# Kernel tuning notes

Measured on AMD Instinct MI355X. Metric: run time of the kernel, lower is better.

## Reference

```python
import jax, jax.numpy as jnp
import numpy as np

B, NV, RN, SN = 1, 4, 1024, 128
H = W = 256
C_FEAT = 32   # img_feat_dim
D_VIEW = 32   # view transformer d_model
PE_D = 8      # PE_d_hid
D_RAY = D_VIEW + PE_D  # 40
NHEAD = 8
EPS_LN = 1e-5


def _layernorm(x, g, b):
    m = x.mean(-1, keepdims=True)
    v = ((x - m) ** 2).mean(-1, keepdims=True)
    return (x - m) * jax.lax.rsqrt(v + EPS_LN) * g + b


def _linear_attention(q, k, v):
    # LoFTR kernelized linear attention; q,k,v: (n, L, h, d)
    Q = jax.nn.elu(q) + 1.0
    K = jax.nn.elu(k) + 1.0
    L = v.shape[1]
    KV = jnp.einsum('nshd,nshv->nhdv', K, v / L)
    Z = 1.0 / (jnp.einsum('nlhd,nhd->nlh', Q, K.sum(axis=1)) + 1e-6)
    return jnp.einsum('nlhd,nhdv,nlh->nlhv', Q, KV, Z) * L


def _loftr_self_layer(x, Wq, Wk, Wv, Wm, g1, b1, W1, W2, g2, b2):
    # LoFTREncoderLayer with self-attention (x is both query and source)
    n, L, d = x.shape
    dim = d // NHEAD
    q = (x @ Wq).reshape(n, L, NHEAD, dim)
    k = (x @ Wk).reshape(n, L, NHEAD, dim)
    v = (x @ Wv).reshape(n, L, NHEAD, dim)
    msg = _linear_attention(q, k, v).reshape(n, L, d) @ Wm
    msg = _layernorm(msg, g1, b1)
    msg = jax.nn.relu(jnp.concatenate([x, msg], -1) @ W1) @ W2
    msg = _layernorm(msg, g2, b2)
    return x + msg


def _grid_sample_2d(img, pix):
    # img: (N,C,H,W); pix: (N,RN,SN,2) in pixel coords.
    # bilinear, align_corners=True, zero padding; mask = in-bounds.
    N, C, Hh, Ww = img.shape
    x, y = pix[..., 0], pix[..., 1]
    mask = ((x >= 0) & (x <= Ww - 1) & (y >= 0) & (y <= Hh - 1)).astype(img.dtype)
    x0 = jnp.floor(x)
    y0 = jnp.floor(y)
    flat = img.reshape(N, C, Hh * Ww)

    def gather(ix, iy):
        valid = ((ix >= 0) & (ix < Ww) & (iy >= 0) & (iy < Hh)).astype(img.dtype)
        idx = (jnp.clip(iy, 0, Hh - 1) * Ww + jnp.clip(ix, 0, Ww - 1)).astype(jnp.int32)
        out = jnp.take_along_axis(flat, idx.reshape(N, 1, -1), axis=2)
        return out.reshape(N, C, ix.shape[1], ix.shape[2]) * valid[:, None]

    wx1 = x - x0
    wy1 = y - y0
    out = (gather(x0, y0) * ((1 - wx1) * (1 - wy1))[:, None]
           + gather(x0 + 1, y0) * (wx1 * (1 - wy1))[:, None]
           + gather(x0, y0 + 1) * ((1 - wx1) * wy1)[:, None]
           + gather(x0 + 1, y0 + 1) * (wx1 * wy1)[:, None])
    return out, mask


def _order_posenc(d_hid, n):
    pos = np.arange(n)[:, None].astype(np.float64)
    j = np.arange(d_hid)[None, :]
    tab = pos / np.power(10000.0, 2 * (j // 2) / d_hid)
    tab[:, 0::2] = np.sin(tab[:, 0::2])
    tab[:, 1::2] = np.cos(tab[:, 1::2])
    return jnp.asarray(tab, dtype=jnp.float32)


def _forward(point3D, source_imgs, source_imgs_feat, ref_pose_inv, source_poses_inv,
             source_poses, view_token,
             vt_Wq, vt_Wk, vt_Wv, vt_Wm, vt_g1, vt_b1, vt_W1, vt_W2, vt_g2, vt_b2,
             rt_Wq, rt_Wk, rt_Wv, rt_Wm, rt_g1, rt_b1, rt_W1, rt_W2, rt_g2, rt_b2,
             dm_W1, dm_b1, dm_W2, dm_b2, dm_W3, dm_b3,
             rw_W1, rw_b1, rw_W2, rw_b2, rw_W3, rw_b3):
    b, nv, _, h, w = source_imgs.shape
    _, rn, sn, _ = point3D.shape

    # relative viewing directions (B,NV,RN,SN,3)
    v1 = point3D - ref_pose_inv[:, None, None, :3, -1]
    v2 = point3D[:, None] - source_poses_inv[:, :, None, None, :3, -1]
    v1 = v1 / jnp.linalg.norm(v1, axis=-1, keepdims=True)
    v2 = v2 / jnp.linalg.norm(v2, axis=-1, keepdims=True)
    dir_relative = v1[:, None] - v2

    # project points into all source views: (B,NV,3,RN,SN)
    pts_h = jnp.concatenate([point3D, jnp.ones_like(point3D[..., :1])], -1)
    pip = jnp.einsum('bnij,brsj->bnirs', source_poses, pts_h)[:, :, :3]
    mask_valid_depth = (pip[:, :, 2] > 0).astype(point3D.dtype)
    pix = pip[:, :, :2] / pip[:, :, 2:3]
    grid = jnp.moveaxis(pix, 2, -1).reshape(b * nv, rn, sn, 2)

    feat_s, mask = _grid_sample_2d(source_imgs_feat.reshape(b * nv, -1, h, w), grid)
    rgb_s, _ = _grid_sample_2d(source_imgs.reshape(b * nv, -1, h, w), grid)
    mask = mask.reshape(b, nv, rn, sn) * mask_valid_depth

    # per-point multi-view tokens: (B*RN*SN, NV, C)
    x = feat_s.reshape(b, nv, -1, rn, sn).transpose(0, 3, 4, 1, 2).reshape(b * rn * sn, nv, -1)
    tok = jnp.broadcast_to(view_token, (x.shape[0], 1, view_token.shape[-1]))
    x = jnp.concatenate([tok, x], axis=1)  # prepend view token -> L = NV+1
    x = _loftr_self_layer(x, vt_Wq, vt_Wk, vt_Wv, vt_Wm, vt_g1, vt_b1, vt_W1, vt_W2, vt_g2, vt_b2)

    x1 = jnp.moveaxis(x, 1, 0)          # (NV+1, B*RN*SN, C)
    view_feature = x1[1:]
    x = x1[0].reshape(b * rn, sn, -1)   # token output per sample along ray

    pe = _order_posenc(PE_D, sn)        # (SN, 8)
    x = jnp.concatenate([x, jnp.broadcast_to(pe, (b * rn, sn, PE_D))], -1)
    x = _loftr_self_layer(x, rt_Wq, rt_Wk, rt_Wv, rt_Wm, rt_g1, rt_b1, rt_W1, rt_W2, rt_g2, rt_b2)

    hdm = jax.nn.relu(x @ dm_W1 + dm_b1)
    hdm = jax.nn.relu(hdm @ dm_W2 + dm_b2)
    srdf = hdm @ dm_W3 + dm_b3           # (B*RN, SN, 1)

    # radiance blending weights over views
    vf = view_feature.reshape(nv, b, rn, sn, -1).transpose(1, 2, 3, 0, 4)  # (B,RN,SN,NV,C)
    dr = dir_relative.transpose(0, 2, 3, 1, 4)                             # (B,RN,SN,NV,3)
    xw = jnp.concatenate([vf, dr], -1)
    xw = jax.nn.relu(xw @ rw_W1 + rw_b1)
    xw = jax.nn.relu(xw @ rw_W2 + rw_b2)
    xw = xw @ rw_W3 + rw_b3                                                # (B,RN,SN,NV,1)
    m = mask.transpose(0, 2, 3, 1)[..., None]
    xw = jnp.where(m == 0, -1e9, xw)
    weight = jax.nn.softmax(xw, axis=-2)
    w_bn = weight[..., 0].transpose(0, 3, 1, 2)[:, :, None]                # (B,NV,1,RN,SN)
    radiance = (rgb_s.reshape(b, nv, 3, rn, sn) * w_bn).sum(axis=1)        # (B,3,RN,SN)
    radiance = radiance.transpose(0, 2, 3, 1).reshape(b * rn * sn, 3)
    return radiance, srdf, pip


def setup_inputs() -> dict:
    key = jax.random.key(0)
    ks = jax.random.split(key, 4)
    u = jax.random.uniform(ks[0], (B, RN, SN, 3), dtype=jnp.float32)
    point3D = jnp.concatenate([u[..., :2] - 0.5, u[..., 2:] + 1.0], -1)  # x,y in [-.5,.5], z in [1,2]
    source_imgs = jax.random.normal(ks[1], (B, NV, 3, H, W), dtype=jnp.float32) * 0.5
    source_imgs_feat = jax.random.normal(ks[2], (B, NV, C_FEAT, H, W), dtype=jnp.float32) * 0.5

    f = 200.0
    P = np.array([[f, 0, W / 2, 0], [0, f, H / 2, 0], [0, 0, 1, 0], [0, 0, 0, 1]], np.float32)
    source_poses = jnp.asarray(np.broadcast_to(P, (B, NV, 4, 4)).copy())
    ref_pose_inv = jnp.asarray(np.broadcast_to(np.eye(4, dtype=np.float32), (B, 4, 4)).copy())
    spi = np.broadcast_to(np.eye(4, dtype=np.float32), (B, NV, 4, 4)).copy()
    spi[:, :, 0, 3] = np.linspace(-0.2, 0.2, NV, dtype=np.float32)  # camera centers
    source_poses_inv = jnp.asarray(spi)

    pk = jax.random.split(ks[3], 20)

    def lin(k, i, o):
        return jax.random.normal(k, (i, o), dtype=jnp.float32) * 0.05

    d, dr = D_VIEW, D_RAY
    params = dict(
        view_token=jax.random.normal(pk[0], (1, d), dtype=jnp.float32),
        vt_Wq=lin(pk[1], d, d), vt_Wk=lin(pk[2], d, d), vt_Wv=lin(pk[3], d, d), vt_Wm=lin(pk[4], d, d),
        vt_g1=jnp.ones(d), vt_b1=jnp.zeros(d),
        vt_W1=lin(pk[5], 2 * d, 2 * d), vt_W2=lin(pk[6], 2 * d, d),
        vt_g2=jnp.ones(d), vt_b2=jnp.zeros(d),
        rt_Wq=lin(pk[7], dr, dr), rt_Wk=lin(pk[8], dr, dr), rt_Wv=lin(pk[9], dr, dr), rt_Wm=lin(pk[10], dr, dr),
        rt_g1=jnp.ones(dr), rt_b1=jnp.zeros(dr),
        rt_W1=lin(pk[11], 2 * dr, 2 * dr), rt_W2=lin(pk[12], 2 * dr, dr),
        rt_g2=jnp.ones(dr), rt_b2=jnp.zeros(dr),
        dm_W1=lin(pk[13], dr, 32), dm_b1=jnp.zeros(32),
        dm_W2=lin(pk[14], 32, 16), dm_b2=jnp.zeros(16),
        dm_W3=lin(pk[15], 16, 1), dm_b3=jnp.zeros(1),
        rw_W1=lin(pk[16], d + 3, 16), rw_b1=jnp.zeros(16),
        rw_W2=lin(pk[17], 16, 8), rw_b2=jnp.zeros(8),
        rw_W3=lin(pk[18], 8, 1), rw_b3=jnp.zeros(1),
    )
    out = dict(point3D=point3D, source_imgs=source_imgs, source_imgs_feat=source_imgs_feat,
               ref_pose_inv=ref_pose_inv, source_poses_inv=source_poses_inv,
               source_poses=source_poses)
    out.update(params)
    return out


def reference(point3D, source_imgs, source_imgs_feat, ref_pose_inv, source_poses_inv,
              source_poses, view_token,
              vt_Wq, vt_Wk, vt_Wv, vt_Wm, vt_g1, vt_b1, vt_W1, vt_W2, vt_g2, vt_b2,
              rt_Wq, rt_Wk, rt_Wv, rt_Wm, rt_g1, rt_b1, rt_W1, rt_W2, rt_g2, rt_b2,
              dm_W1, dm_b1, dm_W2, dm_b2, dm_W3, dm_b3,
              rw_W1, rw_b1, rw_W2, rw_b2, rw_W3, rw_b3):
    return _forward(point3D, source_imgs, source_imgs_feat, ref_pose_inv, source_poses_inv,
                    source_poses, view_token,
                    vt_Wq, vt_Wk, vt_Wv, vt_Wm, vt_g1, vt_b1, vt_W1, vt_W2, vt_g2, vt_b2,
                    rt_Wq, rt_Wk, rt_Wv, rt_Wm, rt_g1, rt_b1, rt_W1, rt_W2, rt_g2, rt_b2,
                    dm_W1, dm_b1, dm_W2, dm_b2, dm_W3, dm_b3,
                    rw_W1, rw_b1, rw_W2, rw_b2, rw_W3, rw_b3)
```

## Files before the change

kernel.cpp:

```cpp
#include <hip/hip_runtime.h>
#include <math.h>

#define NPTS   131072
#define NVIEW  4
#define IMH    256
#define IMW    256

#define WS_FEATT   0u
#define WS_IMGT    8388608u
#define WS_X1      9437184u
#define WS_XR      26214400u
#define WS_MSG     31457280u
#define WS_RGB     36700160u
#define WS_DIR     38273024u
#define WS_MASK    39845888u

__device__ __forceinline__ float elup1(float t) { return t > 0.f ? t + 1.f : expf(t); }

__global__ __launch_bounds__(256) void k0_transpose(
    const float* __restrict__ feat, const float* __restrict__ img,
    float* __restrict__ featT, float* __restrict__ imgT)
{
    int tid = blockIdx.x * 256 + threadIdx.x;
    int v = tid >> 16, pix = tid & 65535;
    float buf[32];
#pragma unroll
    for (int c = 0; c < 32; ++c)
        buf[c] = feat[((size_t)(v * 32 + c) << 16) + pix];
    float4* dst = (float4*)(featT + ((size_t)tid << 5));
#pragma unroll
    for (int q = 0; q < 8; ++q)
        dst[q] = make_float4(buf[4*q], buf[4*q+1], buf[4*q+2], buf[4*q+3]);
    float4 rgb;
    rgb.x = img[((size_t)(v * 3 + 0) << 16) + pix];
    rgb.y = img[((size_t)(v * 3 + 1) << 16) + pix];
    rgb.z = img[((size_t)(v * 3 + 2) << 16) + pix];
    rgb.w = 0.f;
    *(float4*)(imgT + ((size_t)tid << 2)) = rgb;
}

__global__ __launch_bounds__(256) void k1_geom_sample(
    const float* __restrict__ p3d, const float* __restrict__ rpi,
    const float* __restrict__ spi, const float* __restrict__ sp,
    const float* __restrict__ featT, const float* __restrict__ imgT,
    float* __restrict__ x1, float* __restrict__ rgbw,
    float* __restrict__ dirw, float* __restrict__ maskw,
    float* __restrict__ outpip)
{
    int tid = blockIdx.x * 256 + threadIdx.x;
    int p = tid >> 2, v = tid & 3;
    float X = p3d[p * 3 + 0], Y = p3d[p * 3 + 1], Z = p3d[p * 3 + 2];

    float a0 = X - rpi[3], a1 = Y - rpi[7], a2 = Z - rpi[11];
    float na = sqrtf(a0 * a0 + a1 * a1 + a2 * a2);
    a0 /= na; a1 /= na; a2 /= na;
    const float* sv = spi + v * 16;
    float b0 = X - sv[3], b1 = Y - sv[7], b2 = Z - sv[11];
    float nb = sqrtf(b0 * b0 + b1 * b1 + b2 * b2);
    b0 /= nb; b1 /= nb; b2 /= nb;
    dirw[(size_t)p * 12 + v * 3 + 0] = a0 - b0;
    dirw[(size_t)p * 12 + v * 3 + 1] = a1 - b1;
    dirw[(size_t)p * 12 + v * 3 + 2] = a2 - b2;

    const float* P = sp + v * 16;
    float pip0 = P[0] * X + P[1] * Y + P[2]  * Z + P[3];
    float pip1 = P[4] * X + P[5] * Y + P[6]  * Z + P[7];
    float pip2 = P[8] * X + P[9] * Y + P[10] * Z + P[11];
    outpip[(size_t)(v * 3 + 0) * NPTS + p] = pip0;
    outpip[(size_t)(v * 3 + 1) * NPTS + p] = pip1;
    outpip[(size_t)(v * 3 + 2) * NPTS + p] = pip2;

    float gx = pip0 / pip2, gy = pip1 / pip2;
    float inb = (gx >= 0.f && gx <= 255.f && gy >= 0.f && gy <= 255.f) ? 1.f : 0.f;
    float mvd = pip2 > 0.f ? 1.f : 0.f;
    maskw[(size_t)p * 4 + v] = inb * mvd;

    float x0f = floorf(gx), y0f = floorf(gy);
    float wx = gx - x0f, wy = gy - y0f;
    int ix0 = (int)x0f, iy0 = (int)y0f;
    float tw[4] = { (1.f-wx)*(1.f-wy), wx*(1.f-wy), (1.f-wx)*wy, wx*wy };
    int tdx[4] = { 0, 1, 0, 1 };
    int tdy[4] = { 0, 0, 1, 1 };

    float facc[32];
#pragma unroll
    for (int c = 0; c < 32; ++c) facc[c] = 0.f;
    float r0 = 0.f, r1 = 0.f, r2 = 0.f;

#pragma unroll
    for (int tno = 0; tno < 4; ++tno) {
        int ix = ix0 + tdx[tno], iy = iy0 + tdy[tno];
        float valid = (ix >= 0 && ix < IMW && iy >= 0 && iy < IMH) ? 1.f : 0.f;
        int cx = min(max(ix, 0), IMW - 1), cy = min(max(iy, 0), IMH - 1);
        float wgt = tw[tno] * valid;
        size_t base = ((size_t)v << 16) + ((size_t)cy << 8) + (size_t)cx;
        const float4* fp = (const float4*)(featT + base * 32);
#pragma unroll
        for (int q = 0; q < 8; ++q) {
            float4 f4 = fp[q];
            facc[4*q+0] += f4.x * wgt; facc[4*q+1] += f4.y * wgt;
            facc[4*q+2] += f4.z * wgt; facc[4*q+3] += f4.w * wgt;
        }
        float4 rp = *(const float4*)(imgT + base * 4);
        r0 += rp.x * wgt; r1 += rp.y * wgt; r2 += rp.z * wgt;
    }

    float4* xd = (float4*)(x1 + ((size_t)p * 4 + v) * 32);
#pragma unroll
    for (int q = 0; q < 8; ++q)
        xd[q] = make_float4(facc[4*q], facc[4*q+1], facc[4*q+2], facc[4*q+3]);
    rgbw[(size_t)p * 12 + v * 3 + 0] = r0;
    rgbw[(size_t)p * 12 + v * 3 + 1] = r1;
    rgbw[(size_t)p * 12 + v * 3 + 2] = r2;
}

__global__ __launch_bounds__(256) void k2_loftr1(
    float* __restrict__ x1g, const float* __restrict__ vtok,
    const float* __restrict__ Wq, const float* __restrict__ Wk,
    const float* __restrict__ Wv, const float* __restrict__ Wm,
    const float* __restrict__ g1, const float* __restrict__ b1,
    const float* __restrict__ W1, const float* __restrict__ W2,
    const float* __restrict__ g2, const float* __restrict__ b2,
    float* __restrict__ xr)
{
    __shared__ float sm[10400 + 8 * 640];
    int tid = threadIdx.x;
    for (int i = tid; i < 1024; i += 256) {
        sm[i] = Wq[i]; sm[1024 + i] = Wk[i]; sm[2048 + i] = Wv[i]; sm[3072 + i] = Wm[i];
    }
    for (int i = tid; i < 4096; i += 256) sm[4096 + i] = W1[i];
    for (int i = tid; i < 2048; i += 256) sm[8192 + i] = W2[i];
    if (tid < 32) {
        sm[10240 + tid] = g1[tid]; sm[10272 + tid] = b1[tid];
        sm[10304 + tid] = g2[tid]; sm[10336 + tid] = b2[tid];
        sm[10368 + tid] = vtok[tid];
    }
    __syncthreads();

    int pp = tid >> 5, c = tid & 31;
    float* S = sm + 10400 + pp * 640;

    for (int g = blockIdx.x; g < NPTS / 8; g += gridDim.x) {
        int p = g * 8 + pp;
        S[c] = sm[10368 + c];
#pragma unroll
        for (int vv = 0; vv < 4; ++vv)
            S[(1 + vv) * 32 + c] = x1g[((size_t)p * 4 + vv) * 32 + c];
        __syncthreads();

        {
            float qa[5], ka[5], va[5];
#pragma unroll
            for (int l = 0; l < 5; ++l) { qa[l] = 0.f; ka[l] = 0.f; va[l] = 0.f; }
            for (int kk = 0; kk < 32; ++kk) {
                float wq = sm[kk * 32 + c], wk = sm[1024 + kk * 32 + c], wv = sm[2048 + kk * 32 + c];
#pragma unroll
                for (int l = 0; l < 5; ++l) {
                    float xv = S[l * 32 + kk];
                    qa[l] += xv * wq; ka[l] += xv * wk; va[l] += xv * wv;
                }
            }
#pragma unroll
            for (int l = 0; l < 5; ++l) {
                S[160 + l * 32 + c] = elup1(qa[l]);
                S[320 + l * 32 + c] = elup1(ka[l]);
                S[480 + l * 32 + c] = va[l];
            }
        }
        __syncthreads();

        {
            int hb = (c >> 2) << 2;
            float Vl[5], Ke[5][4];
#pragma unroll
            for (int s2 = 0; s2 < 5; ++s2) {
                Vl[s2] = S[480 + s2 * 32 + c];
#pragma unroll
                for (int e = 0; e < 4; ++e) Ke[s2][e] = S[320 + s2 * 32 + hb + e];
            }
            float kv[4] = {0,0,0,0}, ks[4] = {0,0,0,0};
#pragma unroll
            for (int s2 = 0; s2 < 5; ++s2)
#pragma unroll
                for (int e = 0; e < 4; ++e) { kv[e] += Ke[s2][e] * Vl[s2]; ks[e] += Ke[s2][e]; }
#pragma unroll
            for (int l = 0; l < 5; ++l) {
                float q0 = S[160 + l * 32 + hb], q1 = S[160 + l * 32 + hb + 1];
                float q2 = S[160 + l * 32 + hb + 2], q3 = S[160 + l * 32 + hb + 3];
                float den = q0*ks[0] + q1*ks[1] + q2*ks[2] + q3*ks[3] + 1e-6f;
                float o   = q0*kv[0] + q1*kv[1] + q2*kv[2] + q3*kv[3];
                S[480 + l * 32 + c] = o / den;
            }
        }
        __syncthreads();

        {
            float ma[5] = {0,0,0,0,0};
            for (int kk = 0; kk < 32; ++kk) {
                float w = sm[3072 + kk * 32 + c];
#pragma unroll
                for (int l = 0; l < 5; ++l) ma[l] += S[480 + l * 32 + kk] * w;
            }
#pragma unroll
            for (int l = 0; l < 5; ++l) {
                float s1 = ma[l], s2v = ma[l] * ma[l];
#pragma unroll
                for (int off = 16; off > 0; off >>= 1) {
                    s1  += __shfl_xor(s1,  off, 32);
                    s2v += __shfl_xor(s2v, off, 32);
                }
                float m  = s1 * (1.f / 32.f);
                float va = s2v * (1.f / 32.f) - m * m;
                float rs = rsqrtf(va + 1e-5f);
                S[160 + l * 32 + c] = (ma[l] - m) * rs * sm[10240 + c] + sm[10272 + c];
            }
        }
        __syncthreads();

        {
            float hA[5] = {0,0,0,0,0}, hB[5] = {0,0,0,0,0};
            for (int kk = 0; kk < 32; ++kk) {
                float wa = sm[4096 + kk * 64 + c],        wb2 = sm[4096 + kk * 64 + c + 32];
                float wc = sm[4096 + (32 + kk) * 64 + c], wd  = sm[4096 + (32 + kk) * 64 + c + 32];
#pragma unroll
                for (int l = 0; l < 5; ++l) {
                    float xv = S[l * 32 + kk], mv = S[160 + l * 32 + kk];
                    hA[l] += xv * wa + mv * wc;
                    hB[l] += xv * wb2 + mv * wd;
                }
            }
#pragma unroll
            for (int l = 0; l < 5; ++l) {
                S[320 + l * 64 + c]      = fmaxf(hA[l], 0.f);
                S[320 + l * 64 + c + 32] = fmaxf(hB[l], 0.f);
            }
        }
        __syncthreads();

        {
            float oa[5] = {0,0,0,0,0};
            for (int kk = 0; kk < 64; ++kk) {
                float w = sm[8192 + kk * 32 + c];
#pragma unroll
                for (int l = 0; l < 5; ++l) oa[l] += S[320 + l * 64 + kk] * w;
            }
#pragma unroll
            for (int l = 0; l < 5; ++l) {
                float s1 = oa[l], s2v = oa[l] * oa[l];
#pragma unroll
                for (int off = 16; off > 0; off >>= 1) {
                    s1  += __shfl_xor(s1,  off, 32);
                    s2v += __shfl_xor(s2v, off, 32);
                }
                float m  = s1 * (1.f / 32.f);
                float va = s2v * (1.f / 32.f) - m * m;
                float rs = rsqrtf(va + 1e-5f);
                float y  = S[l * 32 + c] + (oa[l] - m) * rs * sm[10304 + c] + sm[10336 + c];
                if (l == 0) xr[(size_t)p * 40 + c] = y;
                else        x1g[((size_t)p * 4 + (l - 1)) * 32 + c] = y;
            }
            if (c < 8) {
                int sidx = p & 127;
                float den = (c < 2) ? 1.f : (c < 4) ? 10.f : (c < 6) ? 100.f : 1000.f;
                float arg = (float)sidx / den;
                xr[(size_t)p * 40 + 32 + c] = (c & 1) ? cosf(arg) : sinf(arg);
            }
        }
        __syncthreads();
    }
}

__global__ __launch_bounds__(320) void k3a_attn(
    const float* __restrict__ xr,
    const float* __restrict__ Wq, const float* __restrict__ Wk,
    const float* __restrict__ Wv, const float* __restrict__ Wm,
    const float* __restrict__ g1, const float* __restrict__ b1,
    float* __restrict__ msg)
{
    __shared__ float kb[5120];
    __shared__ float vb[5120];
    __shared__ float wb[1600];
    __shared__ float kvb[200];
    __shared__ float ksb[40];
    int t = threadIdx.x, r = blockIdx.x;
    const float* xbase = xr + (size_t)r * 5120;
    int lg = t / 40, c = t % 40;

    for (int i = t; i < 1600; i += 320) wb[i] = Wk[i];
    __syncthreads();
    {
        float acc[16];
#pragma unroll
        for (int i = 0; i < 16; ++i) acc[i] = 0.f;
        for (int kk = 0; kk < 40; ++kk) {
            float w = wb[kk * 40 + c];
#pragma unroll
            for (int i = 0; i < 16; ++i) acc[i] += xbase[(lg * 16 + i) * 40 + kk] * w;
        }
#pragma unroll
        for (int i = 0; i < 16; ++i) kb[(lg * 16 + i) * 40 + c] = elup1(acc[i]);
    }
    __syncthreads();
    for (int i = t; i < 1600; i += 320) wb[i] = Wv[i];
    __syncthreads();
    {
        float acc[16];
#pragma unroll
        for (int i = 0; i < 16; ++i) acc[i] = 0.f;
        for (int kk = 0; kk < 40; ++kk) {
            float w = wb[kk * 40 + c];
#pragma unroll
            for (int i = 0; i < 16; ++i) acc[i] += xbase[(lg * 16 + i) * 40 + kk] * w;
        }
#pragma unroll
        for (int i = 0; i < 16; ++i) vb[(lg * 16 + i) * 40 + c] = acc[i];
    }
    __syncthreads();
    if (t < 200) {
        int h = t / 25, e = (t / 5) % 5, d = t % 5;
        float kv = 0.f, ks = 0.f;
        for (int s2 = 0; s2 < 128; ++s2) {
            float kvv = kb[s2 * 40 + h * 5 + e];
            float vv  = vb[s2 * 40 + h * 5 + d];
            kv += kvv * vv; ks += kvv;
        }
        kvb[t] = kv;
        if (d == 0) ksb[h * 5 + e] = ks;
    }
    __syncthreads();
    for (int i = t; i < 1600; i += 320) wb[i] = Wq[i];
    __syncthreads();
    {
        float acc[16];
#pragma unroll
        for (int i = 0; i < 16; ++i) acc[i] = 0.f;
        for (int kk = 0; kk < 40; ++kk) {
            float w = wb[kk * 40 + c];
#pragma unroll
            for (int i = 0; i < 16; ++i) acc[i] += xbase[(lg * 16 + i) * 40 + kk] * w;
        }
#pragma unroll
        for (int i = 0; i < 16; ++i) kb[(lg * 16 + i) * 40 + c] = elup1(acc[i]);
    }
    __syncthreads();
    {
        int h = c / 5, d = c % 5;
#pragma unroll 4
        for (int i = 0; i < 16; ++i) {
            int l = lg * 16 + i;
            float den = 1e-6f, o = 0.f;
#pragma unroll
            for (int e = 0; e < 5; ++e) {
                float q = kb[l * 40 + h * 5 + e];
                den += q * ksb[h * 5 + e];
                o   += q * kvb[h * 25 + e * 5 + d];
            }
            vb[l * 40 + c] = o / den;
        }
    }
    __syncthreads();
    for (int i = t; i < 1600; i += 320) wb[i] = Wm[i];
    __syncthreads();
    {
        float acc[16];
#pragma unroll
        for (int i = 0; i < 16; ++i) acc[i] = 0.f;
        for (int kk = 0; kk < 40; ++kk) {
            float w = wb[kk * 40 + c];
#pragma unroll
            for (int i = 0; i < 16; ++i) acc[i] += vb[(lg * 16 + i) * 40 + kk] * w;
        }
#pragma unroll
        for (int i = 0; i < 16; ++i) kb[(lg * 16 + i) * 40 + c] = acc[i];
    }
    __syncthreads();
    if (t < 128) {
        float s1 = 0.f, s2v = 0.f;
        for (int j = 0; j < 40; ++j) { float x = kb[t * 40 + j]; s1 += x; s2v += x * x; }
        float m = s1 * (1.f / 40.f), va = s2v * (1.f / 40.f) - m * m;
        float rs = rsqrtf(va + 1e-5f);
        for (int j = 0; j < 40; ++j)
            msg[((size_t)r * 128 + t) * 40 + j] = (kb[t * 40 + j] - m) * rs * g1[j] + b1[j];
    }
}

__global__ __launch_bounds__(320) void k3b_ffn(
    float* __restrict__ xr, const float* __restrict__ msg,
    const float* __restrict__ W1, const float* __restrict__ W2,
    const float* __restrict__ g2, const float* __restrict__ b2)
{
    __shared__ float hb[10240];
    __shared__ float wb[3200];
    int t = threadIdx.x, r = blockIdx.x;
    int lg = t / 40, c = t % 40;
    const float* xbase = xr + (size_t)r * 5120;
    const float* mbase = msg + (size_t)r * 5120;

    float hA[16], hB[16];
#pragma unroll
    for (int i = 0; i < 16; ++i) { hA[i] = 0.f; hB[i] = 0.f; }

    for (int i = t; i < 3200; i += 320) wb[i] = W1[i];
    __syncthreads();
    for (int kk = 0; kk < 40; ++kk) {
        float wa = wb[kk * 80 + c], wbb = wb[kk * 80 + c + 40];
#pragma unroll
        for (int i = 0; i < 16; ++i) {
            float xv = xbase[(lg * 16 + i) * 40 + kk];
            hA[i] += xv * wa; hB[i] += xv * wbb;
        }
    }
    __syncthreads();
    for (int i = t; i < 3200; i += 320) wb[i] = W1[3200 + i];
    __syncthreads();
    for (int kk = 0; kk < 40; ++kk) {
        float wa = wb[kk * 80 + c], wbb = wb[kk * 80 + c + 40];
#pragma unroll
        for (int i = 0; i < 16; ++i) {
            float mv = mbase[(lg * 16 + i) * 40 + kk];
            hA[i] += mv * wa; hB[i] += mv * wbb;
        }
    }
#pragma unroll
    for (int i = 0; i < 16; ++i) {
        hb[(lg * 16 + i) * 80 + c]      = fmaxf(hA[i], 0.f);
        hb[(lg * 16 + i) * 80 + c + 40] = fmaxf(hB[i], 0.f);
    }
    __syncthreads();
    for (int i = t; i < 3200; i += 320) wb[i] = W2[i];
    __syncthreads();
    float oa[16];
#pragma unroll
    for (int i = 0; i < 16; ++i) oa[i] = 0.f;
    for (int kk = 0; kk < 80; ++kk) {
        float w = wb[kk * 40 + c];
#pragma unroll
        for (int i = 0; i < 16; ++i) oa[i] += hb[(lg * 16 + i) * 80 + kk] * w;
    }
    __syncthreads();
#pragma unroll
    for (int i = 0; i < 16; ++i) hb[(lg * 16 + i) * 40 + c] = oa[i];
    __syncthreads();
    if (t < 128) {
        float s1 = 0.f, s2v = 0.f;
        for (int j = 0; j < 40; ++j) { float x = hb[t * 40 + j]; s1 += x; s2v += x * x; }
        float m = s1 * (1.f / 40.f), va = s2v * (1.f / 40.f) - m * m;
        float rs = rsqrtf(va + 1e-5f);
        for (int j = 0; j < 40; ++j) {
            float y = xbase[t * 40 + j] + (hb[t * 40 + j] - m) * rs * g2[j] + b2[j];
            xr[(size_t)r * 5120 + t * 40 + j] = y;
        }
    }
}

__global__ __launch_bounds__(256) void k4_dm(
    const float* __restrict__ xr,
    const float* __restrict__ W1, const float* __restrict__ b1,
    const float* __restrict__ W2, const float* __restrict__ b2,
    const float* __restrict__ W3, const float* __restrict__ b3,
    float* __restrict__ out1)
{
    __shared__ float s[1857];
    int t = threadIdx.x;
    for (int i = t; i < 1280; i += 256) s[i] = W1[i];
    if (t < 32) s[1280 + t] = b1[t];
    for (int i = t; i < 512; i += 256) s[1312 + i] = W2[i];
    if (t < 16) { s[1824 + t] = b2[t]; s[1840 + t] = W3[t]; }
    if (t == 0) s[1856] = b3[0];
    __syncthreads();

    int p = blockIdx.x * 256 + t;
    float x[40];
    const float4* xp = (const float4*)(xr + (size_t)p * 40);
#pragma unroll
    for (int i = 0; i < 10; ++i) {
        float4 v4 = xp[i];
        x[4*i] = v4.x; x[4*i+1] = v4.y; x[4*i+2] = v4.z; x[4*i+3] = v4.w;
    }
    float h1[32];
#pragma unroll
    for (int j = 0; j < 32; ++j) h1[j] = s[1280 + j];
    for (int k = 0; k < 40; ++k) {
        float xv = x[k];
#pragma unroll
        for (int j = 0; j < 32; ++j) h1[j] += xv * s[k * 32 + j];
    }
#pragma unroll
    for (int j = 0; j < 32; ++j) h1[j] = fmaxf(h1[j], 0.f);
    float h2[16];
#pragma unroll
    for (int j = 0; j < 16; ++j) h2[j] = s[1824 + j];
    for (int k = 0; k < 32; ++k) {
        float hv = h1[k];
#pragma unroll
        for (int j = 0; j < 16; ++j) h2[j] += hv * s[1312 + k * 16 + j];
    }
    float o = s[1856];
#pragma unroll
    for (int j = 0; j < 16; ++j) o += fmaxf(h2[j], 0.f) * s[1840 + j];
    out1[p] = o;
}

__global__ __launch_bounds__(256) void k5_rw(
    const float* __restrict__ vf, const float* __restrict__ dirw,
    const float* __restrict__ maskw, const float* __restrict__ rgbw,
    const float* __restrict__ W1, const float* __restrict__ b1,
    const float* __restrict__ W2, const float* __restrict__ b2,
    const float* __restrict__ W3, const float* __restrict__ b3,
    float* __restrict__ out0)
{
    __shared__ float s[721];
    int t = threadIdx.x;
    for (int i = t; i < 560; i += 256) s[i] = W1[i];
    if (t < 16) s[560 + t] = b1[t];
    if (t < 128) s[576 + t] = W2[t];
    if (t < 8) { s[704 + t] = b2[t]; s[712 + t] = W3[t]; }
    if (t == 0) s[720] = b3[0];
    __syncthreads();

    int p = blockIdx.x * 256 + t;
    float xw[4];
#pragma unroll
    for (int v = 0; v < 4; ++v) {
        float in[35];
        const float4* vp = (const float4*)(vf + ((size_t)p * 4 + v) * 32);
#pragma unroll
        for (int q = 0; q < 8; ++q) {
            float4 f4 = vp[q];
            in[4*q] = f4.x; in[4*q+1] = f4.y; in[4*q+2] = f4.z; in[4*q+3] = f4.w;
        }
        in[32] = dirw[(size_t)p * 12 + v * 3 + 0];
        in[33] = dirw[(size_t)p * 12 + v * 3 + 1];
        in[34] = dirw[(size_t)p * 12 + v * 3 + 2];
        float h1[16];
#pragma unroll
        for (int j = 0; j < 16; ++j) h1[j] = s[560 + j];
        for (int k = 0; k < 35; ++k) {
            float xv = in[k];
#pragma unroll
            for (int j = 0; j < 16; ++j) h1[j] += xv * s[k * 16 + j];
        }
        float h2[8];
#pragma unroll
        for (int j = 0; j < 8; ++j) h2[j] = s[704 + j];
        for (int k = 0; k < 16; ++k) {
            float hv = fmaxf(h1[k], 0.f);
#pragma unroll
            for (int j = 0; j < 8; ++j) h2[j] += hv * s[576 + k * 8 + j];
        }
        float o = s[720];
#pragma unroll
        for (int j = 0; j < 8; ++j) o += fmaxf(h2[j], 0.f) * s[712 + j];
        xw[v] = (maskw[(size_t)p * 4 + v] == 0.f) ? -1e9f : o;
    }
    float m = fmaxf(fmaxf(xw[0], xw[1]), fmaxf(xw[2], xw[3]));
    float e0 = expf(xw[0] - m), e1 = expf(xw[1] - m), e2 = expf(xw[2] - m), e3 = expf(xw[3] - m);
    float inv = 1.f / (e0 + e1 + e2 + e3);
    float w4[4] = { e0 * inv, e1 * inv, e2 * inv, e3 * inv };
    float r0 = 0.f, r1 = 0.f, r2 = 0.f;
#pragma unroll
    for (int v = 0; v < 4; ++v) {
        r0 += rgbw[(size_t)p * 12 + v * 3 + 0] * w4[v];
        r1 += rgbw[(size_t)p * 12 + v * 3 + 1] * w4[v];
        r2 += rgbw[(size_t)p * 12 + v * 3 + 2] * w4[v];
    }
    out0[(size_t)p * 3 + 0] = r0;
    out0[(size_t)p * 3 + 1] = r1;
    out0[(size_t)p * 3 + 2] = r2;
}

extern "C" void kernel_launch(void* const* d_in, const int* in_sizes, int n_in,
                              void* d_out, int out_size, void* d_ws, size_t ws_size,
                              hipStream_t stream) {
    (void)in_sizes; (void)n_in; (void)out_size; (void)ws_size;
    const float* p3d   = (const float*)d_in[0];
    const float* imgs  = (const float*)d_in[1];
    const float* feat  = (const float*)d_in[2];
    const float* rpi   = (const float*)d_in[3];
    const float* spi   = (const float*)d_in[4];
    const float* sp    = (const float*)d_in[5];
    const float* vtok  = (const float*)d_in[6];
    const float* vtWq  = (const float*)d_in[7];
    const float* vtWk  = (const float*)d_in[8];
    const float* vtWv  = (const float*)d_in[9];
    const float* vtWm  = (const float*)d_in[10];
    const float* vtg1  = (const float*)d_in[11];
    const float* vtb1  = (const float*)d_in[12];
    const float* vtW1  = (const float*)d_in[13];
    const float* vtW2  = (const float*)d_in[14];
    const float* vtg2  = (const float*)d_in[15];
    const float* vtb2  = (const float*)d_in[16];
    const float* rtWq  = (const float*)d_in[17];
    const float* rtWk  = (const float*)d_in[18];
    const float* rtWv  = (const float*)d_in[19];
    const float* rtWm  = (const float*)d_in[20];
    const float* rtg1  = (const float*)d_in[21];
    const float* rtb1  = (const float*)d_in[22];
    const float* rtW1  = (const float*)d_in[23];
    const float* rtW2  = (const float*)d_in[24];
    const float* rtg2  = (const float*)d_in[25];
    const float* rtb2  = (const float*)d_in[26];
    const float* dmW1  = (const float*)d_in[27];
    const float* dmb1  = (const float*)d_in[28];
    const float* dmW2  = (const float*)d_in[29];
    const float* dmb2  = (const float*)d_in[30];
    const float* dmW3  = (const float*)d_in[31];
    const float* dmb3  = (const float*)d_in[32];
    const float* rwW1  = (const float*)d_in[33];
    const float* rwb1  = (const float*)d_in[34];
    const float* rwW2  = (const float*)d_in[35];
    const float* rwb2  = (const float*)d_in[36];
    const float* rwW3  = (const float*)d_in[37];
    const float* rwb3  = (const float*)d_in[38];

    float* out  = (float*)d_out;
    float* out0 = out;
    float* out1 = out + 393216;
    float* out2 = out + 524288;

    float* ws    = (float*)d_ws;
    float* featT = ws + WS_FEATT;
    float* imgT  = ws + WS_IMGT;
    float* x1    = ws + WS_X1;
    float* xr    = ws + WS_XR;
    float* msg   = ws + WS_MSG;
    float* rgbw  = ws + WS_RGB;
    float* dirw  = ws + WS_DIR;
    float* maskw = ws + WS_MASK;

    k0_transpose<<<dim3(1024), dim3(256), 0, stream>>>(feat, imgs, featT, imgT);
    k1_geom_sample<<<dim3(2048), dim3(256), 0, stream>>>(p3d, rpi, spi, sp, featT, imgT,
                                                         x1, rgbw, dirw, maskw, out2);
    k2_loftr1<<<dim3(2048), dim3(256), 0, stream>>>(x1, vtok, vtWq, vtWk, vtWv, vtWm,
                                                    vtg1, vtb1, vtW1, vtW2, vtg2, vtb2, xr);
    k3a_attn<<<dim3(1024), dim3(320), 0, stream>>>(xr, rtWq, rtWk, rtWv, rtWm, rtg1, rtb1, msg);
    k3b_ffn<<<dim3(1024), dim3(320), 0, stream>>>(xr, msg, rtW1, rtW2, rtg2, rtb2);
    k4_dm<<<dim3(512), dim3(256), 0, stream>>>(xr, dmW1, dmb1, dmW2, dmb2, dmW3, dmb3, out1);
    k5_rw<<<dim3(512), dim3(256), 0, stream>>>(x1, dirw, maskw, rgbw,
                                               rwW1, rwb1, rwW2, rwb2, rwW3, rwb3, out0);
}
```

Baseline: 1.219 ms.

## Restructure view-transformer kernel to one token row per thread with register accumulators

The LoFTR view-transformer kernel changes from one point per 32-thread group, with weights staged in shared memory and a barrier between every stage, to a layout where each thread owns one token row (24 points × 5 tokens per 128-thread block). Each thread keeps all 32/64 output channels in registers, and weights are read straight from global memory as uniform values that can go through scalar loads. Layernorm reductions become in-register sums instead of shuffles, and there are far fewer barriers. The cost is heavy register pressure (64-wide accumulators plus q and o arrays) and 8 idle threads per block, which may lower occupancy or cause spills.

```diff
diff --git a/kernel.cpp b/kernel.cpp
--- a/kernel.cpp
+++ b/kernel.cpp
@@ -114,159 +114,276 @@
     rgbw[(size_t)p * 12 + v * 3 + 2] = r2;
 }
 
-__global__ __launch_bounds__(256) void k2_loftr1(
+#define K2_BLK 128
+#define K2_PTS 24
+
+__global__ __launch_bounds__(K2_BLK) void k2_loftr1(
     float* __restrict__ x1g, const float* __restrict__ vtok,
     const float* __restrict__ Wq, const float* __restrict__ Wk,
     const float* __restrict__ Wv, const float* __restrict__ Wm,
-    const float* __restrict__ g1, const float* __restrict__ b1,
+    const float* __restrict__ g1v, const float* __restrict__ b1v,
     const float* __restrict__ W1, const float* __restrict__ W2,
-    const float* __restrict__ g2, const float* __restrict__ b2,
+    const float* __restrict__ g2v, const float* __restrict__ b2v,
     float* __restrict__ xr)
 {
-    __shared__ float sm[10400 + 8 * 640];
-    int tid = threadIdx.x;
-    for (int i = tid; i < 1024; i += 256) {
-        sm[i] = Wq[i]; sm[1024 + i] = Wk[i]; sm[2048 + i] = Wv[i]; sm[3072 + i] = Wm[i];
-    }
-    for (int i = tid; i < 4096; i += 256) sm[4096 + i] = W1[i];
-    for (int i = tid; i < 2048; i += 256) sm[8192 + i] = W2[i];
-    if (tid < 32) {
-        sm[10240 + tid] = g1[tid]; sm[10272 + tid] = b1[tid];
-        sm[10304 + tid] = g2[tid]; sm[10336 + tid] = b2[tid];
-        sm[10368 + tid] = vtok[tid];
-    }
-    __syncthreads();
-
-    int pp = tid >> 5, c = tid & 31;
-    float* S = sm + 10400 + pp * 640;
-
-    for (int g = blockIdx.x; g < NPTS / 8; g += gridDim.x) {
-        int p = g * 8 + pp;
-        S[c] = sm[10368 + c];
-#pragma unroll
-        for (int vv = 0; vv < 4; ++vv)
-            S[(1 + vv) * 32 + c] = x1g[((size_t)p * 4 + vv) * 32 + c];
-        __syncthreads();
-
-        {
-            float qa[5], ka[5], va[5];
-#pragma unroll
-            for (int l = 0; l < 5; ++l) { qa[l] = 0.f; ka[l] = 0.f; va[l] = 0.f; }
-            for (int kk = 0; kk < 32; ++kk) {
-                float wq = sm[kk * 32 + c], wk = sm[1024 + kk * 32 + c], wv = sm[2048 + kk * 32 + c];
-#pragma unroll
-                for (int l = 0; l < 5; ++l) {
-                    float xv = S[l * 32 + kk];
-                    qa[l] += xv * wq; ka[l] += xv * wk; va[l] += xv * wv;
+    __shared__ float xs[8 * K2_BLK * 4];
+    __shared__ float kvs[8192];
+
+    int t = threadIdx.x;
+    int pl = t / 5, l = t - pl * 5;
+    bool act = (t < K2_PTS * 5);
+    if (!act) { pl = 0; l = 0; }
+    int p = blockIdx.x * K2_PTS + pl;
+    bool valid = act && (p < NPTS);
+    int pload = p < NPTS ? p : NPTS - 1;
+
+    {
+        float4 xrow[8];
+        if (l == 0) {
+            const float4* sv = (const float4*)vtok;
+#pragma unroll
+            for (int g = 0; g < 8; ++g) xrow[g] = sv[g];
+        } else {
+            const float4* sv = (const float4*)(x1g + ((size_t)pload * 4 + (l - 1)) * 32);
+#pragma unroll
+            for (int g = 0; g < 8; ++g) xrow[g] = sv[g];
+        }
+#pragma unroll
+        for (int g = 0; g < 8; ++g)
+            *(float4*)&xs[(g * K2_BLK + t) * 4] = xrow[g];
+    }
+
+    {
+        float acc[32];
+#pragma unroll
+        for (int j = 0; j < 32; ++j) acc[j] = 0.f;
+#pragma unroll 2
+        for (int g = 0; g < 8; ++g) {
+            float4 xv = *(const float4*)&xs[(g * K2_BLK + t) * 4];
+            const float* w0 = Wk + g * 128;
+#pragma unroll
+            for (int j = 0; j < 32; ++j) acc[j] = fmaf(xv.x, w0[j],      acc[j]);
+#pragma unroll
+            for (int j = 0; j < 32; ++j) acc[j] = fmaf(xv.y, w0[32 + j], acc[j]);
+#pragma unroll
+            for (int j = 0; j < 32; ++j) acc[j] = fmaf(xv.z, w0[64 + j], acc[j]);
+#pragma unroll
+            for (int j = 0; j < 32; ++j) acc[j] = fmaf(xv.w, w0[96 + j], acc[j]);
+        }
+        if (act) {
+            float* krow = &kvs[(pl * 5 + l) * 68];
+#pragma unroll
+            for (int j = 0; j < 32; j += 4) {
+                float4 o4 = make_float4(elup1(acc[j]), elup1(acc[j+1]), elup1(acc[j+2]), elup1(acc[j+3]));
+                *(float4*)&krow[j] = o4;
+            }
+        }
+#pragma unroll
+        for (int j = 0; j < 32; ++j) acc[j] = 0.f;
+#pragma unroll 2
+        for (int g = 0; g < 8; ++g) {
+            float4 xv = *(const float4*)&xs[(g * K2_BLK + t) * 4];
+            const float* w0 = Wv + g * 128;
+#pragma unroll
+            for (int j = 0; j < 32; ++j) acc[j] = fmaf(xv.x, w0[j],      acc[j]);
+#pragma unroll
+            for (int j = 0; j < 32; ++j) acc[j] = fmaf(xv.y, w0[32 + j], acc[j]);
+#pragma unroll
+            for (int j = 0; j < 32; ++j) acc[j] = fmaf(xv.z, w0[64 + j], acc[j]);
+#pragma unroll
+            for (int j = 0; j < 32; ++j) acc[j] = fmaf(xv.w, w0[96 + j], acc[j]);
+        }
+        if (act) {
+            float* vrow = &kvs[(pl * 5 + l) * 68 + 32];
+#pragma unroll
+            for (int j = 0; j < 32; j += 4)
+                *(float4*)&vrow[j] = make_float4(acc[j], acc[j+1], acc[j+2], acc[j+3]);
+        }
+    }
+
+    float qv[32];
+    {
+        float acc[32];
+#pragma unroll
+        for (int j = 0; j < 32; ++j) acc[j] = 0.f;
+#pragma unroll 2
+        for (int g = 0; g < 8; ++g) {
+            float4 xv = *(const float4*)&xs[(g * K2_BLK + t) * 4];
+            const float* w0 = Wq + g * 128;
+#pragma unroll
+            for (int j = 0; j < 32; ++j) acc[j] = fmaf(xv.x, w0[j],      acc[j]);
+#pragma unroll
+            for (int j = 0; j < 32; ++j) acc[j] = fmaf(xv.y, w0[32 + j], acc[j]);
+#pragma unroll
+            for (int j = 0; j < 32; ++j) acc[j] = fmaf(xv.z, w0[64 + j], acc[j]);
+#pragma unroll
+            for (int j = 0; j < 32; ++j) acc[j] = fmaf(xv.w, w0[96 + j], acc[j]);
+        }
+#pragma unroll
+        for (int j = 0; j < 32; ++j) qv[j] = elup1(acc[j]);
+    }
+    __syncthreads();
+
+    float ov[32];
+    {
+#pragma unroll
+        for (int h = 0; h < 8; ++h) {
+            float kvm[16] = {0,0,0,0,0,0,0,0,0,0,0,0,0,0,0,0};
+            float ksum[4] = {0,0,0,0};
+#pragma unroll
+            for (int l2 = 0; l2 < 5; ++l2) {
+                const float* row = &kvs[(pl * 5 + l2) * 68 + h * 4];
+                float4 K4 = *(const float4*)row;
+                float4 V4 = *(const float4*)(row + 32);
+                kvm[0]  = fmaf(K4.x, V4.x, kvm[0]);  kvm[1]  = fmaf(K4.x, V4.y, kvm[1]);
+                kvm[2]  = fmaf(K4.x, V4.z, kvm[2]);  kvm[3]  = fmaf(K4.x, V4.w, kvm[3]);
+                kvm[4]  = fmaf(K4.y, V4.x, kvm[4]);  kvm[5]  = fmaf(K4.y, V4.y, kvm[5]);
+                kvm[6]  = fmaf(K4.y, V4.z, kvm[6]);  kvm[7]  = fmaf(K4.y, V4.w, kvm[7]);
+                kvm[8]  = fmaf(K4.z, V4.x, kvm[8]);  kvm[9]  = fmaf(K4.z, V4.y, kvm[9]);
+                kvm[10] = fmaf(K4.z, V4.z, kvm[10]); kvm[11] = fmaf(K4.z, V4.w, kvm[11]);
+                kvm[12] = fmaf(K4.w, V4.x, kvm[12]); kvm[13] = fmaf(K4.w, V4.y, kvm[13]);
+                kvm[14] = fmaf(K4.w, V4.z, kvm[14]); kvm[15] = fmaf(K4.w, V4.w, kvm[15]);
+                ksum[0] += K4.x; ksum[1] += K4.y; ksum[2] += K4.z; ksum[3] += K4.w;
+            }
+            float q0 = qv[h*4], q1 = qv[h*4+1], q2 = qv[h*4+2], q3 = qv[h*4+3];
+            float den = 1e-6f + q0*ksum[0] + q1*ksum[1] + q2*ksum[2] + q3*ksum[3];
+            float inv = 1.f / den;
+#pragma unroll
+            for (int d = 0; d < 4; ++d) {
+                float num = q0*kvm[d] + q1*kvm[4+d] + q2*kvm[8+d] + q3*kvm[12+d];
+                ov[h*4+d] = num * inv;
+            }
+        }
+    }
+    __syncthreads();
+
+#pragma unroll
+    for (int g = 0; g < 8; ++g)
+        *(float4*)&kvs[(g * K2_BLK + t) * 4] = make_float4(ov[4*g], ov[4*g+1], ov[4*g+2], ov[4*g+3]);
+
+    float msg[32];
+    {
+        float acc[32];
+#pragma unroll
+        for (int j = 0; j < 32; ++j) acc[j] = 0.f;
+#pragma unroll 2
+        for (int g = 0; g < 8; ++g) {
+            float4 xv = *(const float4*)&kvs[(g * K2_BLK + t) * 4];
+            const float* w0 = Wm + g * 128;
+#pragma unroll
+            for (int j = 0; j < 32; ++j) acc[j] = fmaf(xv.x, w0[j],      acc[j]);
+#pragma unroll
+            for (int j = 0; j < 32; ++j) acc[j] = fmaf(xv.y, w0[32 + j], acc[j]);
+#pragma unroll
+            for (int j = 0; j < 32; ++j) acc[j] = fmaf(xv.z, w0[64 + j], acc[j]);
+#pragma unroll
+            for (int j = 0; j < 32; ++j) acc[j] = fmaf(xv.w, w0[96 + j], acc[j]);
+        }
+        float s1 = 0.f, s2 = 0.f;
+#pragma unroll
+        for (int j = 0; j < 32; ++j) { s1 += acc[j]; s2 += acc[j] * acc[j]; }
+        float m = s1 * (1.f / 32.f);
+        float var = s2 * (1.f / 32.f) - m * m;
+        float rs = rsqrtf(var + 1e-5f);
+#pragma unroll
+        for (int j = 0; j < 32; ++j) msg[j] = (acc[j] - m) * rs * g1v[j] + b1v[j];
+    }
+#pragma unroll
+    for (int g = 0; g < 8; ++g)
+        *(float4*)&kvs[(g * K2_BLK + t) * 4] = make_float4(msg[4*g], msg[4*g+1], msg[4*g+2], msg[4*g+3]);
+
+    {
+        float acc[64];
+#pragma unroll
+        for (int j = 0; j < 64; ++j) acc[j] = 0.f;
+#pragma unroll 2
+        for (int g = 0; g < 8; ++g) {
+            float4 xv = *(const float4*)&xs[(g * K2_BLK + t) * 4];
+            const float* w0 = W1 + g * 256;
+#pragma unroll
+            for (int j = 0; j < 64; ++j) acc[j] = fmaf(xv.x, w0[j],       acc[j]);
+#pragma unroll
+            for (int j = 0; j < 64; ++j) acc[j] = fmaf(xv.y, w0[64 + j],  acc[j]);
+#pragma unroll
+            for (int j = 0; j < 64; ++j) acc[j] = fmaf(xv.z, w0[128 + j], acc[j]);
+#pragma unroll
+            for (int j = 0; j < 64; ++j) acc[j] = fmaf(xv.w, w0[192 + j], acc[j]);
+        }
+#pragma unroll 2
+        for (int g = 0; g < 8; ++g) {
+            float4 xv = *(const float4*)&kvs[(g * K2_BLK + t) * 4];
+            const float* w0 = W1 + 2048 + g * 256;
+#pragma unroll
+            for (int j = 0; j < 64; ++j) acc[j] = fmaf(xv.x, w0[j],       acc[j]);
+#pragma unroll
+            for (int j = 0; j < 64; ++j) acc[j] = fmaf(xv.y, w0[64 + j],  acc[j]);
+#pragma unroll
+            for (int j = 0; j < 64; ++j) acc[j] = fmaf(xv.z, w0[128 + j], acc[j]);
+#pragma unroll
+            for (int j = 0; j < 64; ++j) acc[j] = fmaf(xv.w, w0[192 + j], acc[j]);
+        }
+#pragma unroll
+        for (int g = 0; g < 16; ++g) {
+            float4 h4 = make_float4(fmaxf(acc[4*g], 0.f),   fmaxf(acc[4*g+1], 0.f),
+                                    fmaxf(acc[4*g+2], 0.f), fmaxf(acc[4*g+3], 0.f));
+            *(float4*)&kvs[(g * K2_BLK + t) * 4] = h4;
+        }
+    }
+
+    {
+        float acc[32];
+#pragma unroll
+        for (int j = 0; j < 32; ++j) acc[j] = 0.f;
+#pragma unroll 2
+        for (int g = 0; g < 16; ++g) {
+            float4 xv = *(const float4*)&kvs[(g * K2_BLK + t) * 4];
+            const float* w0 = W2 + g * 128;
+#pragma unroll
+            for (int j = 0; j < 32; ++j) acc[j] = fmaf(xv.x, w0[j],      acc[j]);
+#pragma unroll
+            for (int j = 0; j < 32; ++j) acc[j] = fmaf(xv.y, w0[32 + j], acc[j]);
+#pragma unroll
+            for (int j = 0; j < 32; ++j) acc[j] = fmaf(xv.z, w0[64 + j], acc[j]);
+#pragma unroll
+            for (int j = 0; j < 32; ++j) acc[j] = fmaf(xv.w, w0[96 + j], acc[j]);
+        }
+        float s1 = 0.f, s2 = 0.f;
+#pragma unroll
+        for (int j = 0; j < 32; ++j) { s1 += acc[j]; s2 += acc[j] * acc[j]; }
+        float m = s1 * (1.f / 32.f);
+        float var = s2 * (1.f / 32.f) - m * m;
+        float rs = rsqrtf(var + 1e-5f);
+
+        if (valid) {
+            float y[32];
+#pragma unroll
+            for (int g = 0; g < 8; ++g) {
+                float4 x4 = *(const float4*)&xs[(g * K2_BLK + t) * 4];
+                y[4*g]   = x4.x; y[4*g+1] = x4.y; y[4*g+2] = x4.z; y[4*g+3] = x4.w;
+            }
+#pragma unroll
+            for (int j = 0; j < 32; ++j)
+                y[j] += (acc[j] - m) * rs * g2v[j] + b2v[j];
+
+            if (l == 0) {
+                float4* dst = (float4*)(xr + (size_t)p * 40);
+#pragma unroll
+                for (int g = 0; g < 8; ++g)
+                    dst[g] = make_float4(y[4*g], y[4*g+1], y[4*g+2], y[4*g+3]);
+                int sidx = p & 127;
+#pragma unroll
+                for (int c = 0; c < 8; ++c) {
+                    float den = (c < 2) ? 1.f : (c < 4) ? 10.f : (c < 6) ? 100.f : 1000.f;
+                    float arg = (float)sidx / den;
+                    xr[(size_t)p * 40 + 32 + c] = (c & 1) ? cosf(arg) : sinf(arg);
                 }
+            } else {
+                float4* dst = (float4*)(x1g + ((size_t)p * 4 + (l - 1)) * 32);
+#pragma unroll
+                for (int g = 0; g < 8; ++g)
+                    dst[g] = make_float4(y[4*g], y[4*g+1], y[4*g+2], y[4*g+3]);
             }
-#pragma unroll
-            for (int l = 0; l < 5; ++l) {
-                S[160 + l * 32 + c] = elup1(qa[l]);
-                S[320 + l * 32 + c] = elup1(ka[l]);
-                S[480 + l * 32 + c] = va[l];
-            }
-        }
-        __syncthreads();
-
-        {
-            int hb = (c >> 2) << 2;
-            float Vl[5], Ke[5][4];
-#pragma unroll
-            for (int s2 = 0; s2 < 5; ++s2) {
-                Vl[s2] = S[480 + s2 * 32 + c];
-#pragma unroll
-                for (int e = 0; e < 4; ++e) Ke[s2][e] = S[320 + s2 * 32 + hb + e];
-            }
-            float kv[4] = {0,0,0,0}, ks[4] = {0,0,0,0};
-#pragma unroll
-            for (int s2 = 0; s2 < 5; ++s2)
-#pragma unroll
-                for (int e = 0; e < 4; ++e) { kv[e] += Ke[s2][e] * Vl[s2]; ks[e] += Ke[s2][e]; }
-#pragma unroll
-            for (int l = 0; l < 5; ++l) {
-                float q0 = S[160 + l * 32 + hb], q1 = S[160 + l * 32 + hb + 1];
-                float q2 = S[160 + l * 32 + hb + 2], q3 = S[160 + l * 32 + hb + 3];
-                float den = q0*ks[0] + q1*ks[1] + q2*ks[2] + q3*ks[3] + 1e-6f;
-                float o   = q0*kv[0] + q1*kv[1] + q2*kv[2] + q3*kv[3];
-                S[480 + l * 32 + c] = o / den;
-            }
-        }
-        __syncthreads();
-
-        {
-            float ma[5] = {0,0,0,0,0};
-            for (int kk = 0; kk < 32; ++kk) {
-                float w = sm[3072 + kk * 32 + c];
-#pragma unroll
-                for (int l = 0; l < 5; ++l) ma[l] += S[480 + l * 32 + kk] * w;
-            }
-#pragma unroll
-            for (int l = 0; l < 5; ++l) {
-                float s1 = ma[l], s2v = ma[l] * ma[l];
-#pragma unroll
-                for (int off = 16; off > 0; off >>= 1) {
-                    s1  += __shfl_xor(s1,  off, 32);
-                    s2v += __shfl_xor(s2v, off, 32);
-                }
-                float m  = s1 * (1.f / 32.f);
-                float va = s2v * (1.f / 32.f) - m * m;
-                float rs = rsqrtf(va + 1e-5f);
-                S[160 + l * 32 + c] = (ma[l] - m) * rs * sm[10240 + c] + sm[10272 + c];
-            }
-        }
-        __syncthreads();
-
-        {
-            float hA[5] = {0,0,0,0,0}, hB[5] = {0,0,0,0,0};
-            for (int kk = 0; kk < 32; ++kk) {
-                float wa = sm[4096 + kk * 64 + c],        wb2 = sm[4096 + kk * 64 + c + 32];
-                float wc = sm[4096 + (32 + kk) * 64 + c], wd  = sm[4096 + (32 + kk) * 64 + c + 32];
-#pragma unroll
-                for (int l = 0; l < 5; ++l) {
-                    float xv = S[l * 32 + kk], mv = S[160 + l * 32 + kk];
-                    hA[l] += xv * wa + mv * wc;
-                    hB[l] += xv * wb2 + mv * wd;
-                }
-            }
-#pragma unroll
-            for (int l = 0; l < 5; ++l) {
-                S[320 + l * 64 + c]      = fmaxf(hA[l], 0.f);
-                S[320 + l * 64 + c + 32] = fmaxf(hB[l], 0.f);
-            }
-        }
-        __syncthreads();
-
-        {
-            float oa[5] = {0,0,0,0,0};
-            for (int kk = 0; kk < 64; ++kk) {
-                float w = sm[8192 + kk * 32 + c];
-#pragma unroll
-                for (int l = 0; l < 5; ++l) oa[l] += S[320 + l * 64 + kk] * w;
-            }
-#pragma unroll
-            for (int l = 0; l < 5; ++l) {
-                float s1 = oa[l], s2v = oa[l] * oa[l];
-#pragma unroll
-                for (int off = 16; off > 0; off >>= 1) {
-                    s1  += __shfl_xor(s1,  off, 32);
-                    s2v += __shfl_xor(s2v, off, 32);
-                }
-                float m  = s1 * (1.f / 32.f);
-                float va = s2v * (1.f / 32.f) - m * m;
-                float rs = rsqrtf(va + 1e-5f);
-                float y  = S[l * 32 + c] + (oa[l] - m) * rs * sm[10304 + c] + sm[10336 + c];
-                if (l == 0) xr[(size_t)p * 40 + c] = y;
-                else        x1g[((size_t)p * 4 + (l - 1)) * 32 + c] = y;
-            }
-            if (c < 8) {
-                int sidx = p & 127;
-                float den = (c < 2) ? 1.f : (c < 4) ? 10.f : (c < 6) ? 100.f : 1000.f;
-                float arg = (float)sidx / den;
-                xr[(size_t)p * 40 + 32 + c] = (c & 1) ? cosf(arg) : sinf(arg);
-            }
-        }
-        __syncthreads();
+        }
     }
 }
 
@@ -631,7 +748,8 @@
     k0_transpose<<<dim3(1024), dim3(256), 0, stream>>>(feat, imgs, featT, imgT);
     k1_geom_sample<<<dim3(2048), dim3(256), 0, stream>>>(p3d, rpi, spi, sp, featT, imgT,
                                                          x1, rgbw, dirw, maskw, out2);
-    k2_loftr1<<<dim3(2048), dim3(256), 0, stream>>>(x1, vtok, vtWq, vtWk, vtWv, vtWm,
+    int k2_blocks = (NPTS + K2_PTS - 1) / K2_PTS;
+    k2_loftr1<<<dim3(k2_blocks), dim3(K2_BLK), 0, stream>>>(x1, vtok, vtWq, vtWk, vtWv, vtWm,
                                                     vtg1, vtb1, vtW1, vtW2, vtg2, vtb2, xr);
     k3a_attn<<<dim3(1024), dim3(320), 0, stream>>>(xr, rtWq, rtWk, rtWv, rtWm, rtg1, rtb1, msg);
     k3b_ffn<<<dim3(1024), dim3(320), 0, stream>>>(xr, msg, rtW1, rtW2, rtg2, rtb2);
```

New measurement: 1.252 ms. 1.03x slower.
